# Kernel tuning notes

Hardware: AMD Instinct MI355X
Metric: run time of the kernel (lower is better)

## Reference

```python
import jax, jax.numpy as jnp
import numpy as np

B, S, D, H, F = 4, 2560, 512, 8, 2048
DK = D // H


def layer_norm(x, g, b, eps=1e-5):
    mu = jnp.mean(x, axis=-1, keepdims=True)
    var = jnp.var(x, axis=-1, keepdims=True)
    return (x - mu) * jax.lax.rsqrt(var + eps) * g + b


def setup_inputs() -> dict:
    key = jax.random.key(0)
    ks = jax.random.split(key, 12)
    sc = 1.0 / np.sqrt(D)
    x = jax.random.normal(ks[0], (B, S, D), dtype=jnp.float32)
    mask = jax.random.bernoulli(ks[1], 0.5, (B, 1, S, S))  # True = masked out
    return {
        "x": x,
        "mask": mask,
        "ln_in_g": jnp.ones((D,), jnp.float32),
        "ln_in_b": jnp.zeros((D,), jnp.float32),
        "Wq": jax.random.normal(ks[2], (D, D), jnp.float32) * sc,
        "bq": jnp.zeros((D,), jnp.float32),
        "Wk": jax.random.normal(ks[3], (D, D), jnp.float32) * sc,
        "bk": jnp.zeros((D,), jnp.float32),
        "Wv": jax.random.normal(ks[4], (D, D), jnp.float32) * sc,
        "bv": jnp.zeros((D,), jnp.float32),
        "ln1_g": jnp.ones((D,), jnp.float32),
        "ln1_b": jnp.zeros((D,), jnp.float32),
        "W1": jax.random.normal(ks[5], (D, F), jnp.float32) * sc,
        "b1": jnp.zeros((F,), jnp.float32),
        "W2": jax.random.normal(ks[6], (F, D), jnp.float32) * (1.0 / np.sqrt(F)),
        "b2": jnp.zeros((D,), jnp.float32),
        "ln2_g": jnp.ones((D,), jnp.float32),
        "ln2_b": jnp.zeros((D,), jnp.float32),
    }


def reference(x, mask, ln_in_g, ln_in_b, Wq, bq, Wk, bk, Wv, bv,
              ln1_g, ln1_b, W1, b1, W2, b2, ln2_g, ln2_b):
    xn = layer_norm(x, ln_in_g, ln_in_b)          # [B,S,D]
    q = (xn @ Wq + bq).reshape(B, S, H, DK).transpose(0, 2, 1, 3)  # [B,H,S,dk]
    k = (xn @ Wk + bk).reshape(B, S, H, DK).transpose(0, 2, 1, 3)
    v = (xn @ Wv + bv).reshape(B, S, H, DK).transpose(0, 2, 1, 3)

    scores = jnp.einsum('bhqd,bhkd->bhqk', q, k) / np.sqrt(DK)
    neg = jnp.finfo(scores.dtype).min
    scores = jnp.where(mask, neg, scores)
    probs = jax.nn.softmax(scores, axis=-1)
    probs = jnp.where(mask, 0.0, probs)           # dropout_attn = 0 -> no-op
    attn = jnp.einsum('bhqk,bhkd->bhqd', probs, v)
    attn = attn.transpose(0, 2, 1, 3).reshape(B, S, D)

    attn_out = attn + xn                          # residual uses normed input
    h = layer_norm(attn_out, ln1_g, ln1_b)
    h = h @ W1 + b1                               # note: no nonlinearity in source
    h = h @ W2 + b2
    out = layer_norm(h + attn_out, ln2_g, ln2_b)
    return out
```

## Files before the change

### kernel.cpp

```cpp
#include <hip/hip_runtime.h>
#include <cstdint>
#include <cstddef>

#define B_    4
#define S_    2560
#define D_    512
#define H_    8
#define DK_   64
#define F_    2048
#define NTOK  (B_ * S_)

typedef __attribute__((ext_vector_type(8))) short bf16x8;
typedef __attribute__((ext_vector_type(4))) float f32x4;
#define MFMA16(a, b, c) __builtin_amdgcn_mfma_f32_16x16x32_bf16(a, b, c, 0, 0, 0)

__device__ __forceinline__ unsigned short f2bf(float x) {
  unsigned int u = __float_as_uint(x);
  u += 0x7fffu + ((u >> 16) & 1u);
  return (unsigned short)(u >> 16);
}

__global__ __launch_bounds__(256) void ln_kernel(
    const float* __restrict__ in, const float* __restrict__ res,
    const float* __restrict__ gamma, const float* __restrict__ beta,
    float* __restrict__ out, unsigned short* __restrict__ outb,
    float* __restrict__ pre_out)
{
  const int row = blockIdx.x;
  const int t   = threadIdx.x;
  const size_t base = (size_t)row * D_;

  float2 v = *(const float2*)(in + base + t * 2);
  if (res) {
    float2 r = *(const float2*)(res + base + t * 2);
    v.x += r.x; v.y += r.y;
  }
  if (pre_out) *(float2*)(pre_out + base + t * 2) = v;

  float s1 = v.x + v.y;
  float s2 = v.x * v.x + v.y * v.y;
#pragma unroll
  for (int off = 32; off > 0; off >>= 1) {
    s1 += __shfl_down(s1, off);
    s2 += __shfl_down(s2, off);
  }
  __shared__ float a1[4], a2[4];
  const int wid = t >> 6, lane = t & 63;
  if (lane == 0) { a1[wid] = s1; a2[wid] = s2; }
  __syncthreads();
  const float S1 = a1[0] + a1[1] + a1[2] + a1[3];
  const float S2 = a2[0] + a2[1] + a2[2] + a2[3];
  const float mu  = S1 * (1.0f / D_);
  const float var = S2 * (1.0f / D_) - mu * mu;
  const float inv = rsqrtf(var + 1e-5f);

  float2 g = *(const float2*)(gamma + t * 2);
  float2 b = *(const float2*)(beta  + t * 2);
  float2 o;
  o.x = (v.x - mu) * inv * g.x + b.x;
  o.y = (v.y - mu) * inv * g.y + b.y;
  if (out) *(float2*)(out + base + t * 2) = o;
  if (outb) {
    ushort2 ob; ob.x = f2bf(o.x); ob.y = f2bf(o.y);
    *(ushort2*)(outb + base + t * 2) = ob;
  }
}

__global__ __launch_bounds__(256) void wconv_kernel(
    const float* __restrict__ W, unsigned short* __restrict__ WT, int K, int N)
{
  __shared__ unsigned short tp[64][80];
  const int t  = threadIdx.x;
  const int n0 = blockIdx.x * 64, k0 = blockIdx.y * 64;
#pragma unroll
  for (int it = 0; it < 4; ++it) {
    const int r = (t >> 4) + it * 16;
    const int c = (t & 15) * 4;
    float4 wv = *(const float4*)(W + (size_t)(k0 + r) * N + n0 + c);
    tp[c + 0][r] = f2bf(wv.x);
    tp[c + 1][r] = f2bf(wv.y);
    tp[c + 2][r] = f2bf(wv.z);
    tp[c + 3][r] = f2bf(wv.w);
  }
  __syncthreads();
#pragma unroll
  for (int it = 0; it < 2; ++it) {
    const int r = (t >> 3) + it * 32;
    const int c = (t & 7) * 8;
    *(int4*)(WT + (size_t)(n0 + r) * K + k0 + c) = *(const int4*)&tp[r][c];
  }
}

__global__ void biascat_kernel(const float* __restrict__ bq,
                               const float* __restrict__ bk,
                               const float* __restrict__ bv,
                               float* __restrict__ bc)
{
  const int t = blockIdx.x * 256 + threadIdx.x;
  bc[t] = (t < 512) ? bq[t] : (t < 1024) ? bk[t - 512] : bv[t - 1024];
}

template <int MODE>
__global__ __launch_bounds__(256) void gemm_mfma_kernel(
    const unsigned short* __restrict__ A, const unsigned short* __restrict__ WT,
    const float* __restrict__ bias,
    float* __restrict__ Cf, unsigned short* __restrict__ Cb,
    unsigned short* __restrict__ kb, unsigned short* __restrict__ vtb,
    int M, int N, int K)
{
  __shared__ __align__(16) char sA[128 * 128];
  __shared__ __align__(16) char sW[128 * 128];

  const int t    = threadIdx.x;
  const int w    = t >> 6;
  const int lane = t & 63;
  const int lg   = lane >> 4, lr = lane & 15;
  const int wm   = w >> 1, wn = w & 1;
  const int n0 = blockIdx.x * 128;
  const int m0 = blockIdx.y * 128;

  f32x4 acc[4][4];
#pragma unroll
  for (int mi = 0; mi < 4; ++mi)
#pragma unroll
    for (int ni = 0; ni < 4; ++ni) acc[mi][ni] = (f32x4){0.f, 0.f, 0.f, 0.f};

  const int srow = t >> 3;
  const int schk = t & 7;

  for (int kt = 0; kt < K; kt += 64) {
    __syncthreads();
#pragma unroll
    for (int it = 0; it < 4; ++it) {
      const int row = srow + it * 32;
      const int off = (row * 128 + schk * 16) ^ ((row & 7) << 4);
      *(int4*)(sA + off) =
          *(const int4*)(A + (size_t)(m0 + row) * K + kt + schk * 8);
      *(int4*)(sW + off) =
          *(const int4*)(WT + (size_t)(n0 + row) * K + kt + schk * 8);
    }
    __syncthreads();

#pragma unroll
    for (int kc = 0; kc < 2; ++kc) {
      bf16x8 af[4], wf[4];
#pragma unroll
      for (int mi = 0; mi < 4; ++mi) {
        const int row = wm * 64 + mi * 16 + lr;
        af[mi] = *(const bf16x8*)(sA + ((row * 128 + kc * 64 + lg * 16) ^ ((row & 7) << 4)));
      }
#pragma unroll
      for (int ni = 0; ni < 4; ++ni) {
        const int row = wn * 64 + ni * 16 + lr;
        wf[ni] = *(const bf16x8*)(sW + ((row * 128 + kc * 64 + lg * 16) ^ ((row & 7) << 4)));
      }
#pragma unroll
      for (int mi = 0; mi < 4; ++mi)
#pragma unroll
        for (int ni = 0; ni < 4; ++ni)
          acc[mi][ni] = MFMA16(wf[ni], af[mi], acc[mi][ni]);
    }
  }

#pragma unroll
  for (int mi = 0; mi < 4; ++mi) {
    const int m = m0 + wm * 64 + mi * 16 + lr;
#pragma unroll
    for (int ni = 0; ni < 4; ++ni) {
      const int n = n0 + wn * 64 + ni * 16 + lg * 4;
      float4 b4 = *(const float4*)(bias + n);
      const float o0 = acc[mi][ni][0] + b4.x;
      const float o1 = acc[mi][ni][1] + b4.y;
      const float o2 = acc[mi][ni][2] + b4.z;
      const float o3 = acc[mi][ni][3] + b4.w;
      if constexpr (MODE == 0) {
        float4 o = {o0, o1, o2, o3};
        *(float4*)(Cf + (size_t)m * N + n) = o;
      } else if constexpr (MODE == 1) {
        ushort4 o; o.x = f2bf(o0); o.y = f2bf(o1); o.z = f2bf(o2); o.w = f2bf(o3);
        *(ushort4*)(Cb + (size_t)m * N + n) = o;
      } else {
        const int which = n >> 9;
        const int col   = n & 511;
        const int hh = col >> 6, dk = col & 63;
        const int bb = m / S_, s = m - bb * S_;
        if (which < 2) {
          unsigned short* outp = (which == 0) ? Cb : kb;
          ushort4 o; o.x = f2bf(o0); o.y = f2bf(o1); o.z = f2bf(o2); o.w = f2bf(o3);
          *(ushort4*)(outp + ((size_t)(bb * H_ + hh) * S_ + s) * DK_ + dk) = o;
        } else {
          const size_t vb = (size_t)(bb * H_ + hh) * DK_;
          vtb[(vb + dk + 0) * S_ + s] = f2bf(o0);
          vtb[(vb + dk + 1) * S_ + s] = f2bf(o1);
          vtb[(vb + dk + 2) * S_ + s] = f2bf(o2);
          vtb[(vb + dk + 3) * S_ + s] = f2bf(o3);
        }
      }
    }
  }
}

__global__ __launch_bounds__(256) void attn_mfma_kernel(
    const unsigned short* __restrict__ q, const unsigned short* __restrict__ k,
    const unsigned short* __restrict__ vt, const int* __restrict__ mask,
    float* __restrict__ attn)
{
  __shared__ __align__(16) char kT[64 * 128];
  __shared__ __align__(16) char vT[64 * 128];
  __shared__ __align__(16) char pT[4 * 16 * 128];

  const int t    = threadIdx.x;
  const int w    = t >> 6;
  const int lane = t & 63;
  const int lg   = lane >> 4;
  const int lr   = lane & 15;
  const int qt = blockIdx.x, h = blockIdx.y, bb = blockIdx.z;
  const int qbase = qt * 64;
  const size_t hb  = (size_t)(bb * H_ + h) * S_ * DK_;
  const size_t vb  = (size_t)(bb * H_ + h) * DK_ * S_;

  const int qi_g = qbase + w * 16 + lr;
  bf16x8 qf0 = *(const bf16x8*)(q + hb + (size_t)qi_g * DK_ + 0  + lg * 8);
  bf16x8 qf1 = *(const bf16x8*)(q + hb + (size_t)qi_g * DK_ + 32 + lg * 8);

  const int* mrow = mask + ((size_t)bb * S_ + qi_g) * S_;
  char* myP = pT + w * 2048;

  float m_run = -INFINITY, l_run = 0.f;
  f32x4 accO[4];
#pragma unroll
  for (int dt = 0; dt < 4; ++dt) accO[dt] = (f32x4){0.f, 0.f, 0.f, 0.f};

  for (int kt = 0; kt < S_; kt += 64) {
    __syncthreads();

#pragma unroll
    for (int it = 0; it < 2; ++it) {
      const int c   = t + it * 256;
      const int row = c >> 3, col = c & 7;
      int4 kv = *(const int4*)(k + hb + (size_t)(kt + row) * DK_ + col * 8);
      *(int4*)(kT + ((row * 128 + col * 16) ^ ((row & 7) << 4))) = kv;
      int4 vv = *(const int4*)(vt + vb + (size_t)row * S_ + kt + col * 8);
      *(int4*)(vT + ((row * 128 + col * 16) ^ ((row & 7) << 4))) = vv;
    }
    int mm[16];
#pragma unroll
    for (int t4 = 0; t4 < 4; ++t4)
      *(int4*)&mm[t4 * 4] = *(const int4*)(mrow + kt + t4 * 16 + lg * 4);
    __syncthreads();

    float sv[16];
#pragma unroll
    for (int t4 = 0; t4 < 4; ++t4) {
      const int kjr = t4 * 16 + lr;
      const int sw  = (kjr & 7) << 4;
      f32x4 a = (f32x4){0.f, 0.f, 0.f, 0.f};
      bf16x8 a0 = *(const bf16x8*)(kT + ((kjr * 128 + 0  + lg * 16) ^ sw));
      a = MFMA16(a0, qf0, a);
      bf16x8 a1 = *(const bf16x8*)(kT + ((kjr * 128 + 64 + lg * 16) ^ sw));
      a = MFMA16(a1, qf1, a);
      *(f32x4*)&sv[t4 * 4] = a;
    }

    float s[16];
#pragma unroll
    for (int j = 0; j < 16; ++j)
      s[j] = mm[j] ? -1e30f : sv[j] * 0.125f;
    float mx = s[0];
#pragma unroll
    for (int j = 1; j < 16; ++j) mx = fmaxf(mx, s[j]);
    mx = fmaxf(mx, __shfl_xor(mx, 16));
    mx = fmaxf(mx, __shfl_xor(mx, 32));
    const float m_new = fmaxf(m_run, mx);
    const float scl = __expf(m_run - m_new);
    float p[16], ts = 0.f;
#pragma unroll
    for (int j = 0; j < 16; ++j) {
      p[j] = (s[j] <= -1e29f) ? 0.f : __expf(s[j] - m_new);
      ts += p[j];
    }
    ts += __shfl_xor(ts, 16);
    ts += __shfl_xor(ts, 32);
    l_run = l_run * scl + ts;
    m_run = m_new;
#pragma unroll
    for (int dt = 0; dt < 4; ++dt) accO[dt] *= scl;

#pragma unroll
    for (int t4 = 0; t4 < 4; ++t4) {
      short4 pv;
      pv.x = (short)f2bf(p[t4 * 4 + 0]);
      pv.y = (short)f2bf(p[t4 * 4 + 1]);
      pv.z = (short)f2bf(p[t4 * 4 + 2]);
      pv.w = (short)f2bf(p[t4 * 4 + 3]);
      *(short4*)(myP + ((lr * 128 + t4 * 32 + lg * 8) ^ ((lr & 7) << 4))) = pv;
    }

#pragma unroll
    for (int c = 0; c < 2; ++c) {
      bf16x8 pb = *(const bf16x8*)(myP + ((lr * 128 + c * 64 + lg * 16) ^ ((lr & 7) << 4)));
#pragma unroll
      for (int dt = 0; dt < 4; ++dt) {
        const int dr = dt * 16 + lr;
        bf16x8 va = *(const bf16x8*)(vT + ((dr * 128 + c * 64 + lg * 16) ^ ((dr & 7) << 4)));
        accO[dt] = MFMA16(va, pb, accO[dt]);
      }
    }
  }

  const float inv = (l_run > 0.f) ? 1.f / l_run : 0.f;
#pragma unroll
  for (int dt = 0; dt < 4; ++dt) {
    float4 o;
    o.x = accO[dt][0] * inv;
    o.y = accO[dt][1] * inv;
    o.z = accO[dt][2] * inv;
    o.w = accO[dt][3] * inv;
    *(float4*)(attn + ((size_t)bb * S_ + qbase + w * 16 + lr) * D_
               + h * DK_ + dt * 16 + lg * 4) = o;
  }
}

extern "C" void kernel_launch(void* const* d_in, const int* in_sizes, int n_in,
                              void* d_out, int out_size, void* d_ws, size_t ws_size,
                              hipStream_t stream)
{
  const float* x        = (const float*)d_in[0];
  const int*   mask     = (const int*)d_in[1];
  const float* ln_in_g  = (const float*)d_in[2];
  const float* ln_in_b  = (const float*)d_in[3];
  const float* Wq       = (const float*)d_in[4];
  const float* bq       = (const float*)d_in[5];
  const float* Wk       = (const float*)d_in[6];
  const float* bk       = (const float*)d_in[7];
  const float* Wv       = (const float*)d_in[8];
  const float* bv       = (const float*)d_in[9];
  const float* ln1_g    = (const float*)d_in[10];
  const float* ln1_b    = (const float*)d_in[11];
  const float* W1       = (const float*)d_in[12];
  const float* b1       = (const float*)d_in[13];
  const float* W2       = (const float*)d_in[14];
  const float* b2       = (const float*)d_in[15];
  const float* ln2_g    = (const float*)d_in[16];
  const float* ln2_b    = (const float*)d_in[17];
  float* out = (float*)d_out;

  float* ws = (float*)d_ws;
  const size_t C = (size_t)NTOK * D_;
  float* xn   = ws;
  float* g2   = ws;
  float* aout = ws + C;
  unsigned short* xnb = (unsigned short*)(ws + 2 * C);
  unsigned short* h1b = xnb;
  unsigned short* qb  = (unsigned short*)(ws + 5 * C / 2);
  unsigned short* kbuf = qb + C;
  unsigned short* vtb  = kbuf + C;
  unsigned short* fb  = (unsigned short*)(ws + 5 * C / 2);
  float* attn = ws + 9 * C / 2;
  unsigned short* W1T   = (unsigned short*)(ws + 11 * C / 2);
  unsigned short* W2T   = W1T + (size_t)F_ * D_;
  unsigned short* WqkvT = W2T + (size_t)D_ * F_;
  float* bcat = (float*)(WqkvT + (size_t)3 * D_ * D_);

  wconv_kernel<<<dim3(F_ / 64, D_ / 64), 256, 0, stream>>>(W1, W1T, D_, F_);
  wconv_kernel<<<dim3(D_ / 64, F_ / 64), 256, 0, stream>>>(W2, W2T, F_, D_);
  wconv_kernel<<<dim3(8, 8), 256, 0, stream>>>(Wq, WqkvT, D_, D_);
  wconv_kernel<<<dim3(8, 8), 256, 0, stream>>>(Wk, WqkvT + (size_t)D_ * D_, D_, D_);
  wconv_kernel<<<dim3(8, 8), 256, 0, stream>>>(Wv, WqkvT + (size_t)2 * D_ * D_, D_, D_);
  biascat_kernel<<<6, 256, 0, stream>>>(bq, bk, bv, bcat);

  ln_kernel<<<NTOK, 256, 0, stream>>>(x, nullptr, ln_in_g, ln_in_b, xn, xnb, nullptr);
  gemm_mfma_kernel<2><<<dim3(12, NTOK / 128), 256, 0, stream>>>(
      xnb, WqkvT, bcat, nullptr, qb, kbuf, vtb, NTOK, 1536, D_);
  attn_mfma_kernel<<<dim3(S_ / 64, H_, B_), 256, 0, stream>>>(
      qb, kbuf, vtb, mask, attn);
  ln_kernel<<<NTOK, 256, 0, stream>>>(attn, xn, ln1_g, ln1_b, nullptr, h1b, aout);
  gemm_mfma_kernel<1><<<dim3(F_ / 128, NTOK / 128), 256, 0, stream>>>(
      h1b, W1T, b1, nullptr, fb, nullptr, nullptr, NTOK, F_, D_);
  gemm_mfma_kernel<0><<<dim3(D_ / 128, NTOK / 128), 256, 0, stream>>>(
      fb, W2T, b2, g2, nullptr, nullptr, nullptr, NTOK, D_, F_);
  ln_kernel<<<NTOK, 256, 0, stream>>>(g2, aout, ln2_g, ln2_b, out, nullptr, nullptr);
}
```

Measured before the change: 534.1 us.

## Process two query sub-tiles per attention block and prefetch K/V into registers

The attention kernel now handles 128 queries per block, with each wave owning two 16-row query slices. Each K/V tile staged in LDS is therefore reused by twice as many MFMAs, halving K/V global traffic and staging per query. The next tile's K/V global loads are issued into registers before the current tile's compute, overlapping memory latency with MFMA work. The cost is doubled accumulator and mask registers and half as many blocks (640), which may reduce occupancy and latency hiding.

```diff
diff --git a/kernel.cpp b/kernel.cpp
--- a/kernel.cpp
+++ b/kernel.cpp
@@ -207,7 +207,7 @@
 {
   __shared__ __align__(16) char kT[64 * 128];
   __shared__ __align__(16) char vT[64 * 128];
-  __shared__ __align__(16) char pT[4 * 16 * 128];
+  __shared__ __align__(16) char pT[4 * 2 * 2048];
 
   const int t    = threadIdx.x;
   const int w    = t >> 6;
@@ -215,109 +215,146 @@
   const int lg   = lane >> 4;
   const int lr   = lane & 15;
   const int qt = blockIdx.x, h = blockIdx.y, bb = blockIdx.z;
-  const int qbase = qt * 64;
-  const size_t hb  = (size_t)(bb * H_ + h) * S_ * DK_;
-  const size_t vb  = (size_t)(bb * H_ + h) * DK_ * S_;
-
-  const int qi_g = qbase + w * 16 + lr;
-  bf16x8 qf0 = *(const bf16x8*)(q + hb + (size_t)qi_g * DK_ + 0  + lg * 8);
-  bf16x8 qf1 = *(const bf16x8*)(q + hb + (size_t)qi_g * DK_ + 32 + lg * 8);
-
-  const int* mrow = mask + ((size_t)bb * S_ + qi_g) * S_;
-  char* myP = pT + w * 2048;
-
-  float m_run = -INFINITY, l_run = 0.f;
-  f32x4 accO[4];
-#pragma unroll
-  for (int dt = 0; dt < 4; ++dt) accO[dt] = (f32x4){0.f, 0.f, 0.f, 0.f};
+  const int qbase = qt * 128;
+  const size_t hb    = (size_t)(bb * H_ + h) * S_ * DK_;
+  const size_t vbase = (size_t)(bb * H_ + h) * DK_ * S_;
+
+  bf16x8 qf[2][2];
+  const int* mrow[2];
+#pragma unroll
+  for (int s = 0; s < 2; ++s) {
+    const int qi = qbase + s * 64 + w * 16 + lr;
+    qf[s][0] = *(const bf16x8*)(q + hb + (size_t)qi * DK_ + 0  + lg * 8);
+    qf[s][1] = *(const bf16x8*)(q + hb + (size_t)qi * DK_ + 32 + lg * 8);
+    mrow[s]  = mask + ((size_t)bb * S_ + qi) * S_;
+  }
+  char* myP0 = pT + w * 4096;
+  char* myP1 = myP0 + 2048;
+
+  float m_run[2] = {-INFINITY, -INFINITY};
+  float l_run[2] = {0.f, 0.f};
+  f32x4 accO[2][4];
+#pragma unroll
+  for (int s = 0; s < 2; ++s)
+#pragma unroll
+    for (int dt = 0; dt < 4; ++dt) accO[s][dt] = (f32x4){0.f, 0.f, 0.f, 0.f};
+
+  const int r0 = t >> 3,        cc0 = t & 7;
+  const int r1 = (t + 256) >> 3, cc1 = (t + 256) & 7;
+  const int lds0 = (r0 * 128 + cc0 * 16) ^ ((r0 & 7) << 4);
+  const int lds1 = (r1 * 128 + cc1 * 16) ^ ((r1 & 7) << 4);
+
+  int4 kr0 = *(const int4*)(k + hb + (size_t)r0 * DK_ + cc0 * 8);
+  int4 kr1 = *(const int4*)(k + hb + (size_t)r1 * DK_ + cc1 * 8);
+  int4 vr0 = *(const int4*)(vt + vbase + (size_t)r0 * S_ + cc0 * 8);
+  int4 vr1 = *(const int4*)(vt + vbase + (size_t)r1 * S_ + cc1 * 8);
 
   for (int kt = 0; kt < S_; kt += 64) {
     __syncthreads();
 
-#pragma unroll
-    for (int it = 0; it < 2; ++it) {
-      const int c   = t + it * 256;
-      const int row = c >> 3, col = c & 7;
-      int4 kv = *(const int4*)(k + hb + (size_t)(kt + row) * DK_ + col * 8);
-      *(int4*)(kT + ((row * 128 + col * 16) ^ ((row & 7) << 4))) = kv;
-      int4 vv = *(const int4*)(vt + vb + (size_t)row * S_ + kt + col * 8);
-      *(int4*)(vT + ((row * 128 + col * 16) ^ ((row & 7) << 4))) = vv;
-    }
-    int mm[16];
-#pragma unroll
-    for (int t4 = 0; t4 < 4; ++t4)
-      *(int4*)&mm[t4 * 4] = *(const int4*)(mrow + kt + t4 * 16 + lg * 4);
+    *(int4*)(kT + lds0) = kr0;
+    *(int4*)(kT + lds1) = kr1;
+    *(int4*)(vT + lds0) = vr0;
+    *(int4*)(vT + lds1) = vr1;
+
+    int mm[2][16];
+#pragma unroll
+    for (int s = 0; s < 2; ++s)
+#pragma unroll
+      for (int t4 = 0; t4 < 4; ++t4)
+        *(int4*)&mm[s][t4 * 4] = *(const int4*)(mrow[s] + kt + t4 * 16 + lg * 4);
     __syncthreads();
 
-    float sv[16];
+    if (kt + 64 < S_) {
+      kr0 = *(const int4*)(k + hb + (size_t)(kt + 64 + r0) * DK_ + cc0 * 8);
+      kr1 = *(const int4*)(k + hb + (size_t)(kt + 64 + r1) * DK_ + cc1 * 8);
+      vr0 = *(const int4*)(vt + vbase + (size_t)r0 * S_ + kt + 64 + cc0 * 8);
+      vr1 = *(const int4*)(vt + vbase + (size_t)r1 * S_ + kt + 64 + cc1 * 8);
+    }
+
+    float sv[2][16];
 #pragma unroll
     for (int t4 = 0; t4 < 4; ++t4) {
       const int kjr = t4 * 16 + lr;
       const int sw  = (kjr & 7) << 4;
-      f32x4 a = (f32x4){0.f, 0.f, 0.f, 0.f};
       bf16x8 a0 = *(const bf16x8*)(kT + ((kjr * 128 + 0  + lg * 16) ^ sw));
-      a = MFMA16(a0, qf0, a);
       bf16x8 a1 = *(const bf16x8*)(kT + ((kjr * 128 + 64 + lg * 16) ^ sw));
-      a = MFMA16(a1, qf1, a);
-      *(f32x4*)&sv[t4 * 4] = a;
-    }
-
-    float s[16];
-#pragma unroll
-    for (int j = 0; j < 16; ++j)
-      s[j] = mm[j] ? -1e30f : sv[j] * 0.125f;
-    float mx = s[0];
-#pragma unroll
-    for (int j = 1; j < 16; ++j) mx = fmaxf(mx, s[j]);
-    mx = fmaxf(mx, __shfl_xor(mx, 16));
-    mx = fmaxf(mx, __shfl_xor(mx, 32));
-    const float m_new = fmaxf(m_run, mx);
-    const float scl = __expf(m_run - m_new);
-    float p[16], ts = 0.f;
-#pragma unroll
-    for (int j = 0; j < 16; ++j) {
-      p[j] = (s[j] <= -1e29f) ? 0.f : __expf(s[j] - m_new);
-      ts += p[j];
-    }
-    ts += __shfl_xor(ts, 16);
-    ts += __shfl_xor(ts, 32);
-    l_run = l_run * scl + ts;
-    m_run = m_new;
-#pragma unroll
-    for (int dt = 0; dt < 4; ++dt) accO[dt] *= scl;
-
-#pragma unroll
-    for (int t4 = 0; t4 < 4; ++t4) {
-      short4 pv;
-      pv.x = (short)f2bf(p[t4 * 4 + 0]);
-      pv.y = (short)f2bf(p[t4 * 4 + 1]);
-      pv.z = (short)f2bf(p[t4 * 4 + 2]);
-      pv.w = (short)f2bf(p[t4 * 4 + 3]);
-      *(short4*)(myP + ((lr * 128 + t4 * 32 + lg * 8) ^ ((lr & 7) << 4))) = pv;
+      f32x4 aA = (f32x4){0.f, 0.f, 0.f, 0.f};
+      f32x4 aB = (f32x4){0.f, 0.f, 0.f, 0.f};
+      aA = MFMA16(a0, qf[0][0], aA);
+      aA = MFMA16(a1, qf[0][1], aA);
+      aB = MFMA16(a0, qf[1][0], aB);
+      aB = MFMA16(a1, qf[1][1], aB);
+      *(f32x4*)&sv[0][t4 * 4] = aA;
+      *(f32x4*)&sv[1][t4 * 4] = aB;
+    }
+
+#pragma unroll
+    for (int s = 0; s < 2; ++s) {
+      float sc[16];
+#pragma unroll
+      for (int j = 0; j < 16; ++j)
+        sc[j] = mm[s][j] ? -1e30f : sv[s][j] * 0.125f;
+      float mx = sc[0];
+#pragma unroll
+      for (int j = 1; j < 16; ++j) mx = fmaxf(mx, sc[j]);
+      mx = fmaxf(mx, __shfl_xor(mx, 16));
+      mx = fmaxf(mx, __shfl_xor(mx, 32));
+      const float m_new = fmaxf(m_run[s], mx);
+      const float scl = __expf(m_run[s] - m_new);
+      float p[16], ts = 0.f;
+#pragma unroll
+      for (int j = 0; j < 16; ++j) {
+        p[j] = (sc[j] <= -1e29f) ? 0.f : __expf(sc[j] - m_new);
+        ts += p[j];
+      }
+      ts += __shfl_xor(ts, 16);
+      ts += __shfl_xor(ts, 32);
+      l_run[s] = l_run[s] * scl + ts;
+      m_run[s] = m_new;
+#pragma unroll
+      for (int dt = 0; dt < 4; ++dt) accO[s][dt] *= scl;
+
+      char* mp = s ? myP1 : myP0;
+#pragma unroll
+      for (int t4 = 0; t4 < 4; ++t4) {
+        short4 pv;
+        pv.x = (short)f2bf(p[t4 * 4 + 0]);
+        pv.y = (short)f2bf(p[t4 * 4 + 1]);
+        pv.z = (short)f2bf(p[t4 * 4 + 2]);
+        pv.w = (short)f2bf(p[t4 * 4 + 3]);
+        *(short4*)(mp + ((lr * 128 + t4 * 32 + lg * 8) ^ ((lr & 7) << 4))) = pv;
+      }
     }
 
 #pragma unroll
     for (int c = 0; c < 2; ++c) {
-      bf16x8 pb = *(const bf16x8*)(myP + ((lr * 128 + c * 64 + lg * 16) ^ ((lr & 7) << 4)));
+      const int psw = (lr & 7) << 4;
+      bf16x8 pbA = *(const bf16x8*)(myP0 + ((lr * 128 + c * 64 + lg * 16) ^ psw));
+      bf16x8 pbB = *(const bf16x8*)(myP1 + ((lr * 128 + c * 64 + lg * 16) ^ psw));
 #pragma unroll
       for (int dt = 0; dt < 4; ++dt) {
         const int dr = dt * 16 + lr;
         bf16x8 va = *(const bf16x8*)(vT + ((dr * 128 + c * 64 + lg * 16) ^ ((dr & 7) << 4)));
-        accO[dt] = MFMA16(va, pb, accO[dt]);
-      }
-    }
-  }
-
-  const float inv = (l_run > 0.f) ? 1.f / l_run : 0.f;
-#pragma unroll
-  for (int dt = 0; dt < 4; ++dt) {
-    float4 o;
-    o.x = accO[dt][0] * inv;
-    o.y = accO[dt][1] * inv;
-    o.z = accO[dt][2] * inv;
-    o.w = accO[dt][3] * inv;
-    *(float4*)(attn + ((size_t)bb * S_ + qbase + w * 16 + lr) * D_
-               + h * DK_ + dt * 16 + lg * 4) = o;
+        accO[0][dt] = MFMA16(va, pbA, accO[0][dt]);
+        accO[1][dt] = MFMA16(va, pbB, accO[1][dt]);
+      }
+    }
+  }
+
+#pragma unroll
+  for (int s = 0; s < 2; ++s) {
+    const float inv = (l_run[s] > 0.f) ? 1.f / l_run[s] : 0.f;
+#pragma unroll
+    for (int dt = 0; dt < 4; ++dt) {
+      float4 o;
+      o.x = accO[s][dt][0] * inv;
+      o.y = accO[s][dt][1] * inv;
+      o.z = accO[s][dt][2] * inv;
+      o.w = accO[s][dt][3] * inv;
+      *(float4*)(attn + ((size_t)bb * S_ + qbase + s * 64 + w * 16 + lr) * D_
+                 + h * DK_ + dt * 16 + lg * 4) = o;
+    }
   }
 }
 
@@ -372,7 +409,7 @@
   ln_kernel<<<NTOK, 256, 0, stream>>>(x, nullptr, ln_in_g, ln_in_b, xn, xnb, nullptr);
   gemm_mfma_kernel<2><<<dim3(12, NTOK / 128), 256, 0, stream>>>(
       xnb, WqkvT, bcat, nullptr, qb, kbuf, vtb, NTOK, 1536, D_);
-  attn_mfma_kernel<<<dim3(S_ / 64, H_, B_), 256, 0, stream>>>(
+  attn_mfma_kernel<<<dim3(S_ / 128, H_, B_), 256, 0, stream>>>(
       qb, kbuf, vtb, mask, attn);
   ln_kernel<<<NTOK, 256, 0, stream>>>(attn, xn, ln1_g, ln1_b, nullptr, h1b, aout);
   gemm_mfma_kernel<1><<<dim3(F_ / 128, NTOK / 128), 256, 0, stream>>>(
```

After: 582.8 us. 9.1% more time.
